# Performance work log

Measured on AMD Instinct MI355X. Metric: run time of the kernel, lower is better.

## Reference

```python
import jax, jax.numpy as jnp
import numpy as np

B, L, E, H = 2, 1024, 1024, 16
D = E // H  # head_dim = 64
EPS = 1e-6


def setup_inputs() -> dict:
    key = jax.random.key(0)
    ks = jax.random.split(key, 6)
    x = jax.random.normal(ks[0], (B, L, E), dtype=jnp.float32)
    qkv_w = jax.random.normal(ks[1], (E, 3 * E), dtype=jnp.float32) / np.sqrt(E)
    qkv_b = jnp.zeros((3 * E,), dtype=jnp.float32)
    out_w = jax.random.normal(ks[2], (E, E), dtype=jnp.float32) / np.sqrt(E)
    out_b = jnp.zeros((E,), dtype=jnp.float32)
    norm1_w = jnp.ones((E,), dtype=jnp.float32)
    norm2_w = jnp.ones((E,), dtype=jnp.float32)
    mlp_w1 = jax.random.normal(ks[3], (E, 4 * E), dtype=jnp.float32) / np.sqrt(E)
    mlp_b1 = jnp.zeros((4 * E,), dtype=jnp.float32)
    mlp_w2 = jax.random.normal(ks[4], (4 * E, E), dtype=jnp.float32) / np.sqrt(4 * E)
    mlp_b2 = jnp.zeros((E,), dtype=jnp.float32)
    return dict(x=x, qkv_w=qkv_w, qkv_b=qkv_b, out_w=out_w, out_b=out_b,
                norm1_w=norm1_w, norm2_w=norm2_w,
                mlp_w1=mlp_w1, mlp_b1=mlp_b1, mlp_w2=mlp_w2, mlp_b2=mlp_b2)


def rmsnorm(x, w, eps=1e-6):
    var = jnp.mean(jnp.square(x), axis=-1, keepdims=True)
    return x * jax.lax.rsqrt(var + eps) * w


def cosformer_attn(x, qkv_w, qkv_b, out_w, out_b):
    b, l, e = x.shape
    qkv = x @ qkv_w + qkv_b
    q, k, v = jnp.split(qkv, 3, axis=-1)
    # [B, H, L, D]
    q = q.reshape(b, l, H, D).transpose(0, 2, 1, 3)
    k = k.reshape(b, l, H, D).transpose(0, 2, 1, 3)
    v = v.reshape(b, l, H, D).transpose(0, 2, 1, 3)
    positions = jnp.arange(l, dtype=jnp.float32).reshape(1, 1, l, 1)
    cos_w = jnp.cos(jnp.pi / 2 * positions / l)
    sin_w = jnp.sin(jnp.pi / 2 * positions / l)
    q_prime = jax.nn.relu(q)
    k_prime = jax.nn.relu(k)
    q_cos, q_sin = q_prime * cos_w, q_prime * sin_w
    k_cos, k_sin = k_prime * cos_w, k_prime * sin_w
    # running KV state: cumsum over L of per-position outer products [B,H,L,D,D]
    kv_cos_cumsum = jnp.cumsum(jnp.einsum('bhld,bhle->bhlde', k_cos, v), axis=2)
    context_cos = jnp.einsum('bhld,bhlde->bhle', q_cos, kv_cos_cumsum)
    kv_sin_cumsum = jnp.cumsum(jnp.einsum('bhld,bhle->bhlde', k_sin, v), axis=2)
    context_sin = jnp.einsum('bhld,bhlde->bhle', q_sin, kv_sin_cumsum)
    context = context_cos + context_sin
    k_cos_cumsum = jnp.cumsum(k_cos, axis=2)
    k_sin_cumsum = jnp.cumsum(k_sin, axis=2)
    norm = (jnp.einsum('bhld,bhld->bhl', q_cos, k_cos_cumsum)
            + jnp.einsum('bhld,bhld->bhl', q_sin, k_sin_cumsum))
    output = context / (norm[..., None] + EPS)
    output = output.transpose(0, 2, 1, 3).reshape(b, l, e)
    return output @ out_w + out_b


def reference(x, qkv_w, qkv_b, out_w, out_b, norm1_w, norm2_w,
              mlp_w1, mlp_b1, mlp_w2, mlp_b2):
    # pre-norm transformer block with cosformer causal linear attention
    h = x + cosformer_attn(rmsnorm(x, norm1_w), qkv_w, qkv_b, out_w, out_b)
    m = rmsnorm(h, norm2_w)
    m = jax.nn.gelu(m @ mlp_w1 + mlp_b1) @ mlp_w2 + mlp_b2
    return h + m
```

## Files before the change

kernel.cpp:

```cpp
#include <hip/hip_runtime.h>

#define TB_L 1024
#define TB_E 1024

typedef __attribute__((ext_vector_type(8))) short bf16x8;
typedef __attribute__((ext_vector_type(8))) unsigned short u16x8;
typedef __attribute__((ext_vector_type(4))) float floatx4;

#define AS1(p) ((const __attribute__((address_space(1))) void*)(p))
#define AS3(p) ((__attribute__((address_space(3))) void*)(p))

static __device__ __forceinline__ unsigned short f2bf(float x) {
  union { float f; unsigned u; } c; c.f = x;
  unsigned r = c.u + 0x7fff + ((c.u >> 16) & 1);
  return (unsigned short)(r >> 16);
}
static __device__ __forceinline__ float bf2f(unsigned short h) {
  union { unsigned u; float f; } c; c.u = ((unsigned)h) << 16;
  return c.f;
}
static __device__ __forceinline__ float gelu_f(float x) {
  const float c0 = 0.7978845608028654f;
  const float c1 = 0.044715f;
  float x3 = x * x * x;
  return 0.5f * x * (1.0f + tanhf(c0 * (x + c1 * x3)));
}

static __device__ __forceinline__ int swz(int row, int bytecol) {
  return row * 128 +
         ((((bytecol >> 4) ^ ((row + (row >> 3)) & 7)) << 4) | (bytecol & 15));
}

__global__ __launch_bounds__(256) void rms_kernel(const float* __restrict__ x,
                                                  const float* __restrict__ w,
                                                  unsigned short* __restrict__ out) {
  const int row = blockIdx.x;
  const int tid = threadIdx.x;
  const float4 v = *(const float4*)(x + (size_t)row * TB_E + tid * 4);
  float s = v.x * v.x + v.y * v.y + v.z * v.z + v.w * v.w;
#pragma unroll
  for (int off = 32; off > 0; off >>= 1) s += __shfl_down(s, off);
  __shared__ float red[4];
  if ((tid & 63) == 0) red[tid >> 6] = s;
  __syncthreads();
  const float tot = red[0] + red[1] + red[2] + red[3];
  const float scale = rsqrtf(tot * (1.0f / TB_E) + 1e-6f);
  const float4 wv = *(const float4*)(w + tid * 4);
  ushort4 o;
  o.x = f2bf(v.x * scale * wv.x);
  o.y = f2bf(v.y * scale * wv.y);
  o.z = f2bf(v.z * scale * wv.z);
  o.w = f2bf(v.w * scale * wv.w);
  *(ushort4*)(out + (size_t)row * TB_E + tid * 4) = o;
}

__global__ __launch_bounds__(256) void transpose_bf16(const float* __restrict__ in,
                                                      unsigned short* __restrict__ out,
                                                      int K, int N) {
  __shared__ float t[64][65];
  const int tid = threadIdx.x;
  const int n0 = blockIdx.x * 64, k0 = blockIdx.y * 64;
#pragma unroll
  for (int rep = 0; rep < 4; ++rep) {
    const int r = rep * 16 + (tid >> 4);
    const int c = (tid & 15) * 4;
    const float4 v = *(const float4*)(in + (size_t)(k0 + r) * N + n0 + c);
    t[r][c] = v.x; t[r][c + 1] = v.y; t[r][c + 2] = v.z; t[r][c + 3] = v.w;
  }
  __syncthreads();
#pragma unroll
  for (int rep = 0; rep < 4; ++rep) {
    const int n = rep * 16 + (tid >> 4);
    const int k = (tid & 15) * 4;
    ushort4 o;
    o.x = f2bf(t[k + 0][n]);
    o.y = f2bf(t[k + 1][n]);
    o.z = f2bf(t[k + 2][n]);
    o.w = f2bf(t[k + 3][n]);
    *(ushort4*)(out + (size_t)(n0 + n) * K + k0 + k) = o;
  }
}

template <int BM, int BN, int WM, int WN, bool GELU>
__global__ __launch_bounds__(256) void gemm_bf16(
    const unsigned short* __restrict__ A, const unsigned short* __restrict__ Bt,
    const float* __restrict__ bias, const float* __restrict__ res,
    float* __restrict__ Cf, unsigned short* __restrict__ Cb,
    int M, int N, int K) {
  constexpr int WCOLS = BN / WN;
  constexpr int LA = BM / 64;
  constexpr int LB = BN / 64;
  constexpr int MT = WM / 16;
  constexpr int NT = WN / 16;
  __shared__ __align__(16) unsigned short As[BM * 32];
  __shared__ __align__(16) unsigned short Bs[BN * 32];
  const int tid = threadIdx.x;
  const int wid = tid >> 6, lane = tid & 63;
  const int m0 = blockIdx.y * BM, n0 = blockIdx.x * BN;
  const int mbase = (wid / WCOLS) * WM, nbase = (wid % WCOLS) * WN;

  floatx4 acc[MT][NT];
#pragma unroll
  for (int i = 0; i < MT; ++i)
#pragma unroll
    for (int j = 0; j < NT; ++j) {
      floatx4 z = {0.f, 0.f, 0.f, 0.f};
      acc[i][j] = z;
    }

  const int srow = lane >> 2;
  const int scol = (lane & 3) * 8;
  const unsigned short* Ag = A + (size_t)m0 * K;
  const unsigned short* Bg = Bt + (size_t)n0 * K;
  const char* Ab = (const char*)As;
  const char* Bb = (const char*)Bs;
  const int fr = (lane & 15);
  const int fk = (lane >> 4) * 16;

  for (int k0 = 0; k0 < K; k0 += 32) {
    __syncthreads();
#pragma unroll
    for (int j = 0; j < LA; ++j) {
      const int strip = j * 4 + wid;
      __builtin_amdgcn_global_load_lds(
          AS1(Ag + (size_t)(strip * 16 + srow) * K + k0 + scol),
          AS3((char*)As + strip * 1024), 16, 0, 0);
    }
#pragma unroll
    for (int j = 0; j < LB; ++j) {
      const int strip = j * 4 + wid;
      __builtin_amdgcn_global_load_lds(
          AS1(Bg + (size_t)(strip * 16 + srow) * K + k0 + scol),
          AS3((char*)Bs + strip * 1024), 16, 0, 0);
    }
    __syncthreads();
    bf16x8 af[MT], bfr[NT];
#pragma unroll
    for (int i = 0; i < MT; ++i)
      af[i] = *(const bf16x8*)(Ab + (mbase + i * 16 + fr) * 64 + fk);
#pragma unroll
    for (int j = 0; j < NT; ++j)
      bfr[j] = *(const bf16x8*)(Bb + (nbase + j * 16 + fr) * 64 + fk);
#pragma unroll
    for (int i = 0; i < MT; ++i)
#pragma unroll
      for (int j = 0; j < NT; ++j)
        acc[i][j] = __builtin_amdgcn_mfma_f32_16x16x32_bf16(af[i], bfr[j],
                                                            acc[i][j], 0, 0, 0);
  }

  const int mr = (lane >> 4) * 4;
  const int nc = lane & 15;
#pragma unroll
  for (int i = 0; i < MT; ++i)
#pragma unroll
    for (int j = 0; j < NT; ++j) {
      const int n = n0 + nbase + j * 16 + nc;
      const float bv = bias[n];
#pragma unroll
      for (int r = 0; r < 4; ++r) {
        const int m = m0 + mbase + i * 16 + mr + r;
        float v = acc[i][j][r] + bv;
        if (GELU) v = gelu_f(v);
        if (res) v += res[(size_t)m * N + n];
        if (Cf) Cf[(size_t)m * N + n] = v;
        if (Cb) Cb[(size_t)m * N + n] = f2bf(v);
      }
    }
}

__global__ __launch_bounds__(256) void attn_mfma(const unsigned short* __restrict__ qkv,
                                                 unsigned short* __restrict__ out) {
  const int it = blockIdx.x;
  const int bh = blockIdx.y;
  const int b = bh >> 4, h = bh & 15;
  const int tid = threadIdx.x;
  const int w = tid >> 6, lane = tid & 63;
  const int qd = lane >> 4, ln = lane & 15;
  const int i0 = it * 64;
  __shared__ __align__(16) char sq[8192];
  __shared__ __align__(16) char sk[8192];
  __shared__ __align__(16) char svt[8192];
  __shared__ __align__(16) char ss[8192];
  const unsigned short* base = qkv + (size_t)b * (TB_L * 3072) + h * 64;
  const float PH = 1.5339807878856412e-3f;

#pragma unroll
  for (int p = 0; p < 2; ++p) {
    const int flat = p * 256 + tid;
    const int r = flat >> 3, c = flat & 7;
    u16x8 v = *(const u16x8*)(base + (size_t)(i0 + r) * 3072 + c * 8);
#pragma unroll
    for (int z = 0; z < 8; ++z) v[z] = (v[z] & 0x8000) ? (unsigned short)0 : v[z];
    *(u16x8*)(sq + swz(r, c * 16)) = v;
  }
  __syncthreads();

  bf16x8 aq[2];
#pragma unroll
  for (int ks = 0; ks < 2; ++ks)
    aq[ks] = *(const bf16x8*)(sq + swz(w * 16 + ln, ks * 64 + qd * 16));

  float ci[4], si[4];
#pragma unroll
  for (int r = 0; r < 4; ++r)
    __sincosf(PH * (float)(i0 + w * 16 + qd * 4 + r), &si[r], &ci[r]);

  floatx4 acc_o[4], acc_n;
  {
    floatx4 z = {0.f, 0.f, 0.f, 0.f};
#pragma unroll
    for (int nt = 0; nt < 4; ++nt) acc_o[nt] = z;
    acc_n = z;
  }
  bf16x8 ones;
#pragma unroll
  for (int z = 0; z < 8; ++z) ones[z] = (short)0x3F80;

  for (int jt = 0; jt <= it; ++jt) {
    const int j0 = jt * 64;
    __syncthreads();
#pragma unroll
    for (int p = 0; p < 2; ++p) {
      const int flat = p * 256 + tid;
      const int r = flat >> 3, c = flat & 7;
      u16x8 kv = *(const u16x8*)(base + (size_t)(j0 + r) * 3072 + 1024 + c * 8);
#pragma unroll
      for (int z = 0; z < 8; ++z) kv[z] = (kv[z] & 0x8000) ? (unsigned short)0 : kv[z];
      *(u16x8*)(sk + swz(r, c * 16)) = kv;
      u16x8 vv = *(const u16x8*)(base + (size_t)(j0 + r) * 3072 + 2048 + c * 8);
#pragma unroll
      for (int z = 0; z < 8; ++z)
        *(unsigned short*)(svt + swz(c * 8 + z, r * 2)) = (unsigned short)vv[z];
    }
    __syncthreads();

    floatx4 s_acc[4];
    {
      floatx4 z = {0.f, 0.f, 0.f, 0.f};
#pragma unroll
      for (int nt = 0; nt < 4; ++nt) s_acc[nt] = z;
    }
#pragma unroll
    for (int ks = 0; ks < 2; ++ks)
#pragma unroll
      for (int nt = 0; nt < 4; ++nt) {
        const bf16x8 bk = *(const bf16x8*)(sk + swz(nt * 16 + ln, ks * 64 + qd * 16));
        s_acc[nt] = __builtin_amdgcn_mfma_f32_16x16x32_bf16(aq[ks], bk, s_acc[nt], 0, 0, 0);
      }

    float cj[4], sj[4];
#pragma unroll
    for (int nt = 0; nt < 4; ++nt)
      __sincosf(PH * (float)(j0 + nt * 16 + ln), &sj[nt], &cj[nt]);
    const bool diag = (jt == it);
    const int li = w * 16 + qd * 4;
#pragma unroll
    for (int nt = 0; nt < 4; ++nt) {
      const int jl = nt * 16 + ln;
#pragma unroll
      for (int r = 0; r < 4; ++r) {
        float val = s_acc[nt][r] * (ci[r] * cj[nt] + si[r] * sj[nt]);
        if (diag && jl > li + r) val = 0.f;
        *(unsigned short*)(ss + swz(li + r, jl * 2)) = f2bf(val);
      }
    }

#pragma unroll
    for (int ks = 0; ks < 2; ++ks) {
      const bf16x8 as = *(const bf16x8*)(ss + swz(w * 16 + ln, ks * 64 + qd * 16));
#pragma unroll
      for (int nt = 0; nt < 4; ++nt) {
        const bf16x8 bv = *(const bf16x8*)(svt + swz(nt * 16 + ln, ks * 64 + qd * 16));
        acc_o[nt] = __builtin_amdgcn_mfma_f32_16x16x32_bf16(as, bv, acc_o[nt], 0, 0, 0);
      }
      acc_n = __builtin_amdgcn_mfma_f32_16x16x32_bf16(as, ones, acc_n, 0, 0, 0);
    }
  }

#pragma unroll
  for (int r = 0; r < 4; ++r) {
    const float inv = 1.0f / (acc_n[r] + 1e-6f);
    unsigned short* op =
        out + (size_t)(b * TB_L + i0 + w * 16 + qd * 4 + r) * TB_E + h * 64;
#pragma unroll
    for (int nt = 0; nt < 4; ++nt) op[nt * 16 + ln] = f2bf(acc_o[nt][r] * inv);
  }
}

extern "C" void kernel_launch(void* const* d_in, const int* in_sizes, int n_in,
                              void* d_out, int out_size, void* d_ws, size_t ws_size,
                              hipStream_t stream) {
  const float* x     = (const float*)d_in[0];
  const float* qkv_w = (const float*)d_in[1];
  const float* qkv_b = (const float*)d_in[2];
  const float* out_w = (const float*)d_in[3];
  const float* out_b = (const float*)d_in[4];
  const float* n1w   = (const float*)d_in[5];
  const float* n2w   = (const float*)d_in[6];
  const float* w1    = (const float*)d_in[7];
  const float* b1    = (const float*)d_in[8];
  const float* w2    = (const float*)d_in[9];
  const float* b2    = (const float*)d_in[10];

  char* wsb = (char*)d_ws;
  unsigned short* qkvb  = (unsigned short*)wsb;
  unsigned short* g     = (unsigned short*)wsb;
  unsigned short* xnb   = (unsigned short*)(wsb + 16777216);
  unsigned short* attnb = (unsigned short*)(wsb + 20971520);
  float*          h     = (float*)(wsb + 25165824);
  unsigned short* qkvwt = (unsigned short*)(wsb + 33554432);
  unsigned short* outwt = (unsigned short*)(wsb + 39845888);
  unsigned short* w1t   = (unsigned short*)(wsb + 41943040);
  unsigned short* w2t   = (unsigned short*)(wsb + 50331648);
  float* out = (float*)d_out;
  const int M = 2048;

  transpose_bf16<<<dim3(3072 / 64, 1024 / 64), 256, 0, stream>>>(qkv_w, qkvwt, 1024, 3072);
  transpose_bf16<<<dim3(1024 / 64, 1024 / 64), 256, 0, stream>>>(out_w, outwt, 1024, 1024);
  transpose_bf16<<<dim3(4096 / 64, 1024 / 64), 256, 0, stream>>>(w1, w1t, 1024, 4096);
  transpose_bf16<<<dim3(1024 / 64, 4096 / 64), 256, 0, stream>>>(w2, w2t, 4096, 1024);

  rms_kernel<<<dim3(M), 256, 0, stream>>>(x, n1w, xnb);
  gemm_bf16<64, 128, 64, 32, false><<<dim3(3072 / 128, M / 64), 256, 0, stream>>>(
      xnb, qkvwt, qkv_b, nullptr, nullptr, qkvb, M, 3072, 1024);
  attn_mfma<<<dim3(16, 32), 256, 0, stream>>>(qkvb, attnb);
  gemm_bf16<64, 64, 32, 32, false><<<dim3(1024 / 64, M / 64), 256, 0, stream>>>(
      attnb, outwt, out_b, x, h, nullptr, M, 1024, 1024);
  rms_kernel<<<dim3(M), 256, 0, stream>>>(h, n2w, xnb);
  gemm_bf16<128, 128, 64, 64, true><<<dim3(4096 / 128, M / 128), 256, 0, stream>>>(
      xnb, w1t, b1, nullptr, nullptr, g, M, 4096, 1024);
  gemm_bf16<64, 64, 32, 32, false><<<dim3(1024 / 64, M / 64), 256, 0, stream>>>(
      g, w2t, b2, h, out, nullptr, M, 1024, 4096);
}
```

Before: 302.4 us.

## Merge weight transposes into one launch and retune GEMM tiles with BK parameter

The four weight-transpose launches become a single kernel that picks its matrix from the block index, saving launch overhead. The GEMM gains a BK template parameter so one LDS stage can hold several 32-wide K chunks, which halves the barriers for the down-projection with BK=64. The QKV and output-projection GEMMs move to larger 128-row tiles for more operand reuse, at the cost of fewer blocks in flight and more LDS per block.

```diff
diff --git a/kernel.cpp b/kernel.cpp
--- a/kernel.cpp
+++ b/kernel.cpp
@@ -54,12 +54,21 @@
   *(ushort4*)(out + (size_t)row * TB_E + tid * 4) = o;
 }
 
-__global__ __launch_bounds__(256) void transpose_bf16(const float* __restrict__ in,
-                                                      unsigned short* __restrict__ out,
-                                                      int K, int N) {
+__global__ __launch_bounds__(256) void transpose_all(
+    const float* __restrict__ s0, const float* __restrict__ s1,
+    const float* __restrict__ s2, const float* __restrict__ s3,
+    unsigned short* __restrict__ d0, unsigned short* __restrict__ d1,
+    unsigned short* __restrict__ d2, unsigned short* __restrict__ d3) {
+  const int id = blockIdx.x;
+  const float* in; unsigned short* out; int K, N, lid;
+  if (id < 768)       { in = s0; out = d0; K = 1024; N = 3072; lid = id; }
+  else if (id < 1024) { in = s1; out = d1; K = 1024; N = 1024; lid = id - 768; }
+  else if (id < 2048) { in = s2; out = d2; K = 1024; N = 4096; lid = id - 1024; }
+  else                { in = s3; out = d3; K = 4096; N = 1024; lid = id - 2048; }
+  const int nx = N >> 6;
+  const int n0 = (lid % nx) * 64, k0 = (lid / nx) * 64;
   __shared__ float t[64][65];
   const int tid = threadIdx.x;
-  const int n0 = blockIdx.x * 64, k0 = blockIdx.y * 64;
 #pragma unroll
   for (int rep = 0; rep < 4; ++rep) {
     const int r = rep * 16 + (tid >> 4);
@@ -81,19 +90,22 @@
   }
 }
 
-template <int BM, int BN, int WM, int WN, bool GELU>
+template <int BM, int BN, int BK, int WM, int WN, bool GELU>
 __global__ __launch_bounds__(256) void gemm_bf16(
     const unsigned short* __restrict__ A, const unsigned short* __restrict__ Bt,
     const float* __restrict__ bias, const float* __restrict__ res,
     float* __restrict__ Cf, unsigned short* __restrict__ Cb,
     int M, int N, int K) {
+  constexpr int KC = BK / 32;
   constexpr int WCOLS = BN / WN;
-  constexpr int LA = BM / 64;
-  constexpr int LB = BN / 64;
   constexpr int MT = WM / 16;
   constexpr int NT = WN / 16;
-  __shared__ __align__(16) unsigned short As[BM * 32];
-  __shared__ __align__(16) unsigned short Bs[BN * 32];
+  constexpr int ACH = (BM / 16) * KC;
+  constexpr int BCH = (BN / 16) * KC;
+  static_assert((BM / WM) * (BN / WN) == 4, "4 waves");
+  static_assert(ACH % 4 == 0 && BCH % 4 == 0, "chunks divisible by waves");
+  __shared__ __align__(16) unsigned short As[BM * BK];
+  __shared__ __align__(16) unsigned short Bs[BN * BK];
   const int tid = threadIdx.x;
   const int wid = tid >> 6, lane = tid & 63;
   const int m0 = blockIdx.y * BM, n0 = blockIdx.x * BN;
@@ -117,36 +129,43 @@
   const int fr = (lane & 15);
   const int fk = (lane >> 4) * 16;
 
-  for (int k0 = 0; k0 < K; k0 += 32) {
+  for (int k0 = 0; k0 < K; k0 += BK) {
     __syncthreads();
 #pragma unroll
-    for (int j = 0; j < LA; ++j) {
-      const int strip = j * 4 + wid;
+    for (int j = 0; j < ACH / 4; ++j) {
+      const int ch = j * 4 + wid;
+      const int strip = ch / KC, half = ch % KC;
       __builtin_amdgcn_global_load_lds(
-          AS1(Ag + (size_t)(strip * 16 + srow) * K + k0 + scol),
-          AS3((char*)As + strip * 1024), 16, 0, 0);
-    }
-#pragma unroll
-    for (int j = 0; j < LB; ++j) {
-      const int strip = j * 4 + wid;
+          AS1(Ag + (size_t)(strip * 16 + srow) * K + k0 + half * 32 + scol),
+          AS3((char*)As + ch * 1024), 16, 0, 0);
+    }
+#pragma unroll
+    for (int j = 0; j < BCH / 4; ++j) {
+      const int ch = j * 4 + wid;
+      const int strip = ch / KC, half = ch % KC;
       __builtin_amdgcn_global_load_lds(
-          AS1(Bg + (size_t)(strip * 16 + srow) * K + k0 + scol),
-          AS3((char*)Bs + strip * 1024), 16, 0, 0);
+          AS1(Bg + (size_t)(strip * 16 + srow) * K + k0 + half * 32 + scol),
+          AS3((char*)Bs + ch * 1024), 16, 0, 0);
     }
     __syncthreads();
-    bf16x8 af[MT], bfr[NT];
-#pragma unroll
-    for (int i = 0; i < MT; ++i)
-      af[i] = *(const bf16x8*)(Ab + (mbase + i * 16 + fr) * 64 + fk);
-#pragma unroll
-    for (int j = 0; j < NT; ++j)
-      bfr[j] = *(const bf16x8*)(Bb + (nbase + j * 16 + fr) * 64 + fk);
-#pragma unroll
-    for (int i = 0; i < MT; ++i)
+#pragma unroll
+    for (int g = 0; g < KC; ++g) {
+      bf16x8 af[MT], bfr[NT];
+#pragma unroll
+      for (int i = 0; i < MT; ++i)
+        af[i] = *(const bf16x8*)(Ab + ((mbase / 16 + i) * KC + g) * 1024 +
+                                 fr * 64 + fk);
 #pragma unroll
       for (int j = 0; j < NT; ++j)
-        acc[i][j] = __builtin_amdgcn_mfma_f32_16x16x32_bf16(af[i], bfr[j],
-                                                            acc[i][j], 0, 0, 0);
+        bfr[j] = *(const bf16x8*)(Bb + ((nbase / 16 + j) * KC + g) * 1024 +
+                                  fr * 64 + fk);
+#pragma unroll
+      for (int i = 0; i < MT; ++i)
+#pragma unroll
+        for (int j = 0; j < NT; ++j)
+          acc[i][j] = __builtin_amdgcn_mfma_f32_16x16x32_bf16(af[i], bfr[j],
+                                                              acc[i][j], 0, 0, 0);
+    }
   }
 
   const int mr = (lane >> 4) * 4;
@@ -316,20 +335,18 @@
   float* out = (float*)d_out;
   const int M = 2048;
 
-  transpose_bf16<<<dim3(3072 / 64, 1024 / 64), 256, 0, stream>>>(qkv_w, qkvwt, 1024, 3072);
-  transpose_bf16<<<dim3(1024 / 64, 1024 / 64), 256, 0, stream>>>(out_w, outwt, 1024, 1024);
-  transpose_bf16<<<dim3(4096 / 64, 1024 / 64), 256, 0, stream>>>(w1, w1t, 1024, 4096);
-  transpose_bf16<<<dim3(1024 / 64, 4096 / 64), 256, 0, stream>>>(w2, w2t, 4096, 1024);
+  transpose_all<<<dim3(3072), 256, 0, stream>>>(qkv_w, out_w, w1, w2,
+                                                qkvwt, outwt, w1t, w2t);
 
   rms_kernel<<<dim3(M), 256, 0, stream>>>(x, n1w, xnb);
-  gemm_bf16<64, 128, 64, 32, false><<<dim3(3072 / 128, M / 64), 256, 0, stream>>>(
+  gemm_bf16<128, 128, 32, 64, 64, false><<<dim3(3072 / 128, M / 128), 256, 0, stream>>>(
       xnb, qkvwt, qkv_b, nullptr, nullptr, qkvb, M, 3072, 1024);
   attn_mfma<<<dim3(16, 32), 256, 0, stream>>>(qkvb, attnb);
-  gemm_bf16<64, 64, 32, 32, false><<<dim3(1024 / 64, M / 64), 256, 0, stream>>>(
+  gemm_bf16<128, 64, 32, 64, 32, false><<<dim3(1024 / 64, M / 128), 256, 0, stream>>>(
       attnb, outwt, out_b, x, h, nullptr, M, 1024, 1024);
   rms_kernel<<<dim3(M), 256, 0, stream>>>(h, n2w, xnb);
-  gemm_bf16<128, 128, 64, 64, true><<<dim3(4096 / 128, M / 128), 256, 0, stream>>>(
+  gemm_bf16<128, 128, 32, 64, 64, true><<<dim3(4096 / 128, M / 128), 256, 0, stream>>>(
       xnb, w1t, b1, nullptr, nullptr, g, M, 4096, 1024);
-  gemm_bf16<64, 64, 32, 32, false><<<dim3(1024 / 64, M / 64), 256, 0, stream>>>(
+  gemm_bf16<128, 64, 64, 64, 32, false><<<dim3(1024 / 64, M / 128), 256, 0, stream>>>(
       g, w2t, b2, h, out, nullptr, M, 1024, 4096);
 }
```

New measurement: 314.1 us. +3.9%, slower.
